# Performance work log

Hardware: AMD Instinct MI355X
Metric: run time of the kernel (lower is better)

## Reference

```python
import jax, jax.numpy as jnp
import numpy as np

N = 100000   # nodes
E = 1600000  # edges (avg degree 16)
D_IN = 128
H = 256
D_OUT = 128


def setup_inputs() -> dict:
    key = jax.random.key(0)
    ks = jax.random.split(key, 12)

    def lin_w(k, fan_in, fan_out):
        # torch nn.Linear-style uniform init
        bound = 1.0 / np.sqrt(fan_in)
        return jax.random.uniform(k, (fan_in, fan_out), jnp.float32, -bound, bound)

    return {
        "in_feat": jax.random.normal(ks[0], (N, D_IN), jnp.float32),
        "src": jax.random.randint(ks[1], (E,), 0, N, jnp.int32),
        "dst": jax.random.randint(ks[2], (E,), 0, N, jnp.int32),
        "Wc0": lin_w(ks[3], D_IN, H), "bc0": jnp.zeros((H,), jnp.float32),
        "Wc1": lin_w(ks[4], H, H),    "bc1": jnp.zeros((H,), jnp.float32),
        "Wc2": lin_w(ks[5], H, D_OUT),"bc2": jnp.zeros((D_OUT,), jnp.float32),
        "Wr0": lin_w(ks[6], D_OUT, H),"br0": jnp.zeros((H,), jnp.float32),
        "Wr1": lin_w(ks[7], H, H),    "br1": jnp.zeros((H,), jnp.float32),
        "Wr2": lin_w(ks[8], H, D_IN), "br2": jnp.zeros((D_IN,), jnp.float32),
    }


def _graph_conv(h, src, dst, W, b):
    """DGL GraphConv, norm='both': D_out^{-1/2} A D_in^{-1/2} h W + b."""
    ones = jnp.ones(src.shape[0], h.dtype)
    out_deg = jnp.clip(jax.ops.segment_sum(ones, src, num_segments=N), 1.0)
    in_deg = jnp.clip(jax.ops.segment_sum(ones, dst, num_segments=N), 1.0)
    h = h * (out_deg ** -0.5)[:, None]
    h = h @ W                                    # transform before aggregate
    h = jax.ops.segment_sum(h[src], dst, num_segments=N)  # SpMM aggregation
    return h * (in_deg ** -0.5)[:, None] + b


def reference(in_feat, src, dst, Wc0, bc0, Wc1, bc1, Wc2, bc2,
              Wr0, br0, Wr1, br1, Wr2, br2):
    h = jnp.tanh(_graph_conv(in_feat, src, dst, Wc0, bc0))
    h = jnp.tanh(_graph_conv(h, src, dst, Wc1, bc1))
    h = jax.nn.softmax(_graph_conv(h, src, dst, Wc2, bc2), axis=1)
    r = jnp.tanh(h @ Wr0 + br0)
    r = jnp.tanh(r @ Wr1 + br1)
    r = jax.nn.softmax(r @ Wr2 + br2, axis=1)
    return (h, r)
```

## Files before the change

kernel.cpp:

```cpp
#include <hip/hip_runtime.h>

typedef __attribute__((ext_vector_type(8))) short short8;
typedef __attribute__((ext_vector_type(4))) float f32x4;

__device__ __forceinline__ ushort f2bf(float v) {
    unsigned u = __builtin_bit_cast(unsigned, v);
    unsigned r = (u + 0x7FFFu + ((u >> 16) & 1u)) >> 16;
    return (ushort)r;
}
__device__ __forceinline__ float lo16(unsigned p) { return __builtin_bit_cast(float, p << 16); }
__device__ __forceinline__ float hi16(unsigned p) { return __builtin_bit_cast(float, p & 0xFFFF0000u); }

__device__ __forceinline__ float fast_tanh(float x) {
    float cx = fminf(fmaxf(x, -9.f), 9.f);
    float e = __expf(2.f * cx);
    return (e - 1.f) / (e + 1.f);
}

__device__ __forceinline__ void async16(const void* g, void* l) {
    __builtin_amdgcn_global_load_lds(
        (const __attribute__((address_space(1))) unsigned*)g,
        (__attribute__((address_space(3))) unsigned*)l, 16, 0, 0);
}

#define BSHIFT 9
#define CHUNK 4096

__global__ __launch_bounds__(256) void bucket_count(const int* __restrict__ src,
        const int* __restrict__ dst, int* __restrict__ gbc,
        int* __restrict__ outc, int E) {
    __shared__ int cnt[256];
    int t = threadIdx.x;
    cnt[t] = 0;
    __syncthreads();
    int start = blockIdx.x * CHUNK;
    int n = E - start; if (n > CHUNK) n = CHUNK;
#pragma unroll
    for (int k = 0; k < CHUNK / 256; ++k) {
        int i = t + k * 256;
        if (i < n) {
            atomicAdd(&cnt[dst[start + i] >> BSHIFT], 1);
            atomicAdd(&outc[src[start + i]], 1);
        }
    }
    __syncthreads();
    if (cnt[t]) atomicAdd(&gbc[t], cnt[t]);
}

__global__ void scan_buckets(const int* __restrict__ gbc, int* __restrict__ bucketBase,
                             int* __restrict__ pairCursor, int* __restrict__ roff,
                             int N, int E) {
    __shared__ int s[256];
    int t = threadIdx.x;
    int v = gbc[t];
    s[t] = v; __syncthreads();
    for (int o = 1; o < 256; o <<= 1) {
        int y = (t >= o) ? s[t - o] : 0;
        __syncthreads();
        s[t] += y;
        __syncthreads();
    }
    int excl = s[t] - v;
    bucketBase[t] = excl;
    pairCursor[t] = excl;
    if (t == 255) bucketBase[256] = s[255];
    if (t == 0) roff[N] = E;
}

__global__ __launch_bounds__(256) void part_scatter(const int* __restrict__ src,
        const int* __restrict__ dst, int* __restrict__ pairCursor,
        uint2* __restrict__ pairs, int E) {
    __shared__ int cnt[256];
    __shared__ int base[256];
    int t = threadIdx.x;
    cnt[t] = 0;
    __syncthreads();
    int start = blockIdx.x * CHUNK;
    int n = E - start; if (n > CHUNK) n = CHUNK;
    int sv[CHUNK / 256], dv[CHUNK / 256], rk[CHUNK / 256], bk[CHUNK / 256];
#pragma unroll
    for (int k = 0; k < CHUNK / 256; ++k) {
        int i = t + k * 256;
        if (i < n) {
            sv[k] = src[start + i];
            dv[k] = dst[start + i];
            bk[k] = dv[k] >> BSHIFT;
            rk[k] = atomicAdd(&cnt[bk[k]], 1);
        } else bk[k] = -1;
    }
    __syncthreads();
    base[t] = cnt[t] ? atomicAdd(&pairCursor[t], cnt[t]) : 0;
    __syncthreads();
#pragma unroll
    for (int k = 0; k < CHUNK / 256; ++k)
        if (bk[k] >= 0) pairs[base[bk[k]] + rk[k]] = make_uint2((unsigned)sv[k], (unsigned)dv[k]);
}

__global__ __launch_bounds__(256) void build_bucket(const uint2* __restrict__ pairs,
        const int* __restrict__ bucketBase, int* __restrict__ roff,
        float* __restrict__ sIn, int* __restrict__ csr, int N) {
    __shared__ int cnt[512];
    __shared__ int cur[512];
    __shared__ int ss[256];
    int b = blockIdx.x;
    int t = threadIdx.x;
    int lo = b << BSHIFT;
    int s0 = bucketBase[b], s1 = bucketBase[b + 1];
    cnt[t] = 0; cnt[t + 256] = 0;
    __syncthreads();
    for (int j = s0 + t; j < s1; j += 256)
        atomicAdd(&cnt[pairs[j].y - lo], 1);
    __syncthreads();
    int c0 = cnt[2 * t], c1 = cnt[2 * t + 1];
    ss[t] = c0 + c1; __syncthreads();
    for (int o = 1; o < 256; o <<= 1) {
        int y = (t >= o) ? ss[t - o] : 0;
        __syncthreads();
        ss[t] += y;
        __syncthreads();
    }
    int eb = ss[t] - (c0 + c1);
    int p0 = s0 + eb, p1 = s0 + eb + c0;
    cur[2 * t] = p0; cur[2 * t + 1] = p1;
    int n0 = lo + 2 * t, n1 = n0 + 1;
    if (n0 < N) { roff[n0] = p0; sIn[n0] = rsqrtf((float)(c0 > 0 ? c0 : 1)); }
    if (n1 < N) { roff[n1] = p1; sIn[n1] = rsqrtf((float)(c1 > 0 ? c1 : 1)); }
    __syncthreads();
    for (int j = s0 + t; j < s1; j += 256) {
        uint2 p = pairs[j];
        int pos = atomicAdd(&cur[p.y - lo], 1);
        csr[pos] = (int)p.x;
    }
}

__global__ void convw(const float* w0, const float* w1, const float* w2,
                      const float* w3, const float* w4, const float* w5,
                      ushort* __restrict__ Wt) {
    int i = blockIdx.x * 256 + threadIdx.x;
    int base, Km, Nm; const float* W;
    if      (i < 32768)  { base = 0;      Km = 128; Nm = 256; W = w0; }
    else if (i < 98304)  { base = 32768;  Km = 256; Nm = 256; W = w1; }
    else if (i < 131072) { base = 98304;  Km = 256; Nm = 128; W = w2; }
    else if (i < 163840) { base = 131072; Km = 128; Nm = 256; W = w3; }
    else if (i < 229376) { base = 163840; Km = 256; Nm = 256; W = w4; }
    else                 { base = 229376; Km = 256; Nm = 128; W = w5; }
    int l = i - base;
    int k = l / Nm, n = l % Nm;
    Wt[base + n * Km + k] = f2bf(W[l]);
}

__global__ void prescale(const float* __restrict__ x, const int* __restrict__ outc,
                         ushort* __restrict__ o, float* __restrict__ sOut,
                         int total ) {
    int i = blockIdx.x * 256 + threadIdx.x;
    if (i >= total) return;
    int row = i >> 5;
    int oc = outc[row]; if (oc < 1) oc = 1;
    float s = rsqrtf((float)oc);
    if ((i & 31) == 0) sOut[row] = s;
    float4 v = ((const float4*)x)[i];
    ushort4 r;
    r.x = f2bf(v.x * s); r.y = f2bf(v.y * s);
    r.z = f2bf(v.z * s); r.w = f2bf(v.w * s);
    ((ushort4*)o)[i] = r;
}

__global__ __launch_bounds__(256) void agg128(const ushort* __restrict__ F,
        const int* __restrict__ csr, const int* __restrict__ roff,
        const float* __restrict__ sIn, ushort* __restrict__ out, int N) {
    int w = blockIdx.x * 4 + (threadIdx.x >> 6);
    if (w >= N) return;
    int lane = threadIdx.x & 63;
    int b = roff[w], e = roff[w + 1];
    float a0 = 0.f, a1 = 0.f;
    const ushort* base = F + lane * 2;
    int i = b;
    for (; i + 4 <= e; i += 4) {
        int s0 = csr[i], s1 = csr[i + 1], s2 = csr[i + 2], s3 = csr[i + 3];
        unsigned p0 = *(const unsigned*)(base + (size_t)s0 * 128);
        unsigned p1 = *(const unsigned*)(base + (size_t)s1 * 128);
        unsigned p2 = *(const unsigned*)(base + (size_t)s2 * 128);
        unsigned p3 = *(const unsigned*)(base + (size_t)s3 * 128);
        a0 += lo16(p0) + lo16(p1) + lo16(p2) + lo16(p3);
        a1 += hi16(p0) + hi16(p1) + hi16(p2) + hi16(p3);
    }
    for (; i < e; ++i) {
        unsigned p = *(const unsigned*)(base + (size_t)csr[i] * 128);
        a0 += lo16(p); a1 += hi16(p);
    }
    float s = sIn[w];
    ushort2 o2; o2.x = f2bf(a0 * s); o2.y = f2bf(a1 * s);
    *(ushort2*)(out + (size_t)w * 128 + lane * 2) = o2;
}

__global__ __launch_bounds__(256) void agg256(const ushort* __restrict__ F,
        const int* __restrict__ csr, const int* __restrict__ roff,
        const float* __restrict__ sIn, ushort* __restrict__ out, int N) {
    int w = blockIdx.x * 4 + (threadIdx.x >> 6);
    if (w >= N) return;
    int lane = threadIdx.x & 63;
    int b = roff[w], e = roff[w + 1];
    float a0 = 0.f, a1 = 0.f, a2 = 0.f, a3 = 0.f;
    const ushort* base = F + lane * 4;
    int i = b;
    for (; i + 4 <= e; i += 4) {
        int s0 = csr[i], s1 = csr[i + 1], s2 = csr[i + 2], s3 = csr[i + 3];
        uint2 p0 = *(const uint2*)(base + (size_t)s0 * 256);
        uint2 p1 = *(const uint2*)(base + (size_t)s1 * 256);
        uint2 p2 = *(const uint2*)(base + (size_t)s2 * 256);
        uint2 p3 = *(const uint2*)(base + (size_t)s3 * 256);
        a0 += lo16(p0.x) + lo16(p1.x) + lo16(p2.x) + lo16(p3.x);
        a1 += hi16(p0.x) + hi16(p1.x) + hi16(p2.x) + hi16(p3.x);
        a2 += lo16(p0.y) + lo16(p1.y) + lo16(p2.y) + lo16(p3.y);
        a3 += hi16(p0.y) + hi16(p1.y) + hi16(p2.y) + hi16(p3.y);
    }
    for (; i < e; ++i) {
        uint2 p = *(const uint2*)(base + (size_t)csr[i] * 256);
        a0 += lo16(p.x); a1 += hi16(p.x); a2 += lo16(p.y); a3 += hi16(p.y);
    }
    float s = sIn[w];
    ushort4 o4;
    o4.x = f2bf(a0 * s); o4.y = f2bf(a1 * s);
    o4.z = f2bf(a2 * s); o4.w = f2bf(a3 * s);
    *(ushort4*)(out + (size_t)w * 256 + lane * 4) = o4;
}

__global__ __launch_bounds__(256) void agg_softmax(const ushort* __restrict__ F,
        const int* __restrict__ csr, const int* __restrict__ roff,
        const float* __restrict__ sIn, const float* __restrict__ bias,
        float* __restrict__ outh, ushort* __restrict__ outb, int N) {
    int w = blockIdx.x * 4 + (threadIdx.x >> 6);
    if (w >= N) return;
    int lane = threadIdx.x & 63;
    int b = roff[w], e = roff[w + 1];
    float a0 = 0.f, a1 = 0.f;
    const ushort* base = F + lane * 2;
    int i = b;
    for (; i + 4 <= e; i += 4) {
        int s0 = csr[i], s1 = csr[i + 1], s2 = csr[i + 2], s3 = csr[i + 3];
        unsigned p0 = *(const unsigned*)(base + (size_t)s0 * 128);
        unsigned p1 = *(const unsigned*)(base + (size_t)s1 * 128);
        unsigned p2 = *(const unsigned*)(base + (size_t)s2 * 128);
        unsigned p3 = *(const unsigned*)(base + (size_t)s3 * 128);
        a0 += lo16(p0) + lo16(p1) + lo16(p2) + lo16(p3);
        a1 += hi16(p0) + hi16(p1) + hi16(p2) + hi16(p3);
    }
    for (; i < e; ++i) {
        unsigned p = *(const unsigned*)(base + (size_t)csr[i] * 128);
        a0 += lo16(p); a1 += hi16(p);
    }
    float s = sIn[w];
    float2 bb = *(const float2*)(bias + lane * 2);
    float l0 = a0 * s + bb.x, l1 = a1 * s + bb.y;
    float m = fmaxf(l0, l1);
    for (int o = 32; o; o >>= 1) m = fmaxf(m, __shfl_xor(m, o, 64));
    float e0 = __expf(l0 - m), e1 = __expf(l1 - m);
    float sm = e0 + e1;
    for (int o = 32; o; o >>= 1) sm += __shfl_xor(sm, o, 64);
    float inv = 1.f / sm;
    float r0 = e0 * inv, r1 = e1 * inv;
    float2 fo; fo.x = r0; fo.y = r1;
    *(float2*)(outh + (size_t)w * 128 + lane * 2) = fo;
    ushort2 o2; o2.x = f2bf(r0); o2.y = f2bf(r1);
    *(ushort2*)(outb + (size_t)w * 128 + lane * 2) = o2;
}

__global__ __launch_bounds__(256) void softmax_r(const float* __restrict__ L,
                                                 float* __restrict__ out, int N) {
    int w = blockIdx.x * 4 + (threadIdx.x >> 6);
    if (w >= N) return;
    int lane = threadIdx.x & 63;
    const float* row = L + (size_t)w * 128;
    float l0 = row[lane], l1 = row[lane + 64];
    float m = fmaxf(l0, l1);
    for (int o = 32; o; o >>= 1) m = fmaxf(m, __shfl_xor(m, o, 64));
    float e0 = __expf(l0 - m), e1 = __expf(l1 - m);
    float sm = e0 + e1;
    for (int o = 32; o; o >>= 1) sm += __shfl_xor(sm, o, 64);
    float inv = 1.f / sm;
    out[(size_t)w * 128 + lane] = e0 * inv;
    out[(size_t)w * 128 + 64 + lane] = e1 * inv;
}

template <int MODE>
__global__ __launch_bounds__(256) void gemm_kernel(
        const ushort* __restrict__ A, const ushort* __restrict__ Wt,
        const float* __restrict__ bias, const float* __restrict__ rowscale,
        void* __restrict__ out, int M, int K, int Nn) {
    __shared__ ushort ldsA[128 * 64];
    __shared__ ushort ldsB[128 * 64];
    const int tid = threadIdx.x;
    const int lane = tid & 63;
    const int wid = tid >> 6;
    const int rowbase = blockIdx.x * 128;
    const int colbase = blockIdx.y * 128;
    const int wr = (wid >> 1) * 64;
    const int wc = (wid & 1) * 64;

    f32x4 acc[4][4];
#pragma unroll
    for (int i = 0; i < 4; ++i)
#pragma unroll
        for (int j = 0; j < 4; ++j) acc[i][j] = (f32x4){0.f, 0.f, 0.f, 0.f};

    const int sr = lane >> 3;
    const int sp = lane & 7;

    for (int kt = 0; kt < K; kt += 64) {
        __syncthreads();
#pragma unroll
        for (int it = 0; it < 4; ++it) {
            int rl = wid * 32 + it * 8 + sr;
            int grow = rowbase + rl; if (grow > M - 1) grow = M - 1;
            int gca = kt + ((sp ^ (rl & 7)) << 3);
            async16(A + (size_t)grow * K + gca, (char*)ldsA + (wid * 32 + it * 8) * 128);
            int gn = colbase + rl;
            int gcb = kt + ((sp ^ (rl & 7)) << 3);
            async16(Wt + (size_t)gn * K + gcb, (char*)ldsB + (wid * 32 + it * 8) * 128);
        }
        __syncthreads();
        const int l15 = lane & 15, l4 = lane >> 4;
#pragma unroll
        for (int ks = 0; ks < 2; ++ks) {
            short8 af[4], bfr[4];
#pragma unroll
            for (int rt = 0; rt < 4; ++rt) {
                int r = wr + rt * 16 + l15;
                int slot = (ks * 4 + l4) ^ (r & 7);
                af[rt] = *(const short8*)&ldsA[r * 64 + slot * 8];
            }
#pragma unroll
            for (int ct = 0; ct < 4; ++ct) {
                int n = wc + ct * 16 + l15;
                int slot = (ks * 4 + l4) ^ (n & 7);
                bfr[ct] = *(const short8*)&ldsB[n * 64 + slot * 8];
            }
#pragma unroll
            for (int rt = 0; rt < 4; ++rt)
#pragma unroll
                for (int ct = 0; ct < 4; ++ct)
                    acc[rt][ct] = __builtin_amdgcn_mfma_f32_16x16x32_bf16(
                        af[rt], bfr[ct], acc[rt][ct], 0, 0, 0);
        }
    }

    const int l15 = lane & 15, l4 = lane >> 4;
    float bv[4];
#pragma unroll
    for (int ct = 0; ct < 4; ++ct)
        bv[ct] = (MODE != 1 && bias) ? bias[colbase + wc + ct * 16 + l15] : 0.f;
#pragma unroll
    for (int rt = 0; rt < 4; ++rt) {
#pragma unroll
        for (int rg = 0; rg < 4; ++rg) {
            int row = rowbase + wr + rt * 16 + l4 * 4 + rg;
            if (row >= M) continue;
            float sc = 1.f;
            if (MODE == 0 && rowscale) sc = rowscale[row];
#pragma unroll
            for (int ct = 0; ct < 4; ++ct) {
                int col = colbase + wc + ct * 16 + l15;
                float v = acc[rt][ct][rg] + bv[ct];
                if (MODE == 0) v = fast_tanh(v) * sc;
                if (MODE <= 1)
                    ((ushort*)out)[(size_t)row * Nn + col] = f2bf(v);
                else
                    ((float*)out)[(size_t)row * Nn + col] = v;
            }
        }
    }
}

extern "C" void kernel_launch(void* const* d_in, const int* in_sizes, int n_in,
                              void* d_out, int out_size, void* d_ws, size_t ws_size,
                              hipStream_t stream) {
    (void)n_in; (void)out_size; (void)ws_size;
    const float* in_feat = (const float*)d_in[0];
    const int*   src     = (const int*)d_in[1];
    const int*   dstp    = (const int*)d_in[2];
    const float* Wc0 = (const float*)d_in[3];  const float* bc0 = (const float*)d_in[4];
    const float* Wc1 = (const float*)d_in[5];  const float* bc1 = (const float*)d_in[6];
    const float* Wc2 = (const float*)d_in[7];  const float* bc2 = (const float*)d_in[8];
    const float* Wr0 = (const float*)d_in[9];  const float* br0 = (const float*)d_in[10];
    const float* Wr1 = (const float*)d_in[11]; const float* br1 = (const float*)d_in[12];
    const float* Wr2 = (const float*)d_in[13]; const float* br2 = (const float*)d_in[14];

    const int N = in_sizes[0] / 128;
    const int E = in_sizes[1];
    const int numBuckets = (N + ((1 << BSHIFT) - 1)) >> BSHIFT;

    char* ws = (char*)d_ws;
    size_t off = 0;
    auto alloc = [&](size_t bytes) -> char* {
        char* p = ws + off;
        off += (bytes + 255) & ~(size_t)255;
        return p;
    };
    char* S1 = alloc((size_t)N * 256 * 2);
    char* S2 = alloc((size_t)N * 256 * 2);
    int* csr    = (int*)alloc((size_t)E * 4);
    int* roff   = (int*)alloc((size_t)(N + 1) * 4);
    int* outc   = (int*)alloc((size_t)N * 4);
    float* sOut = (float*)alloc((size_t)N * 4);
    float* sIn  = (float*)alloc((size_t)N * 4);
    ushort* Wt  = (ushort*)alloc(262144 * 2);
    int* gbc        = (int*)alloc(256 * 4);
    int* bucketBase = (int*)alloc(257 * 4);
    int* pairCursor = (int*)alloc(256 * 4);
    uint2* pairs = (uint2*)S2;

    hipMemsetAsync(outc, 0, (size_t)N * 4, stream);
    hipMemsetAsync(gbc, 0, 256 * 4, stream);

    int nblk = (E + CHUNK - 1) / CHUNK;
    bucket_count<<<nblk, 256, 0, stream>>>(src, dstp, gbc, outc, E);
    scan_buckets<<<1, 256, 0, stream>>>(gbc, bucketBase, pairCursor, roff, N, E);
    part_scatter<<<nblk, 256, 0, stream>>>(src, dstp, pairCursor, pairs, E);
    build_bucket<<<numBuckets, 256, 0, stream>>>(pairs, bucketBase, roff, sIn, csr, N);

    convw<<<262144 / 256, 256, 0, stream>>>(Wc0, Wc1, Wc2, Wr0, Wr1, Wr2, Wt);

    ushort* Xs = (ushort*)S1;
    prescale<<<(N * 32 + 255) / 256, 256, 0, stream>>>(in_feat, outc, Xs, sOut, N * 32);

    int aggGrid = (N + 3) / 4;
    dim3 g2((N + 127) / 128, 2), g1((N + 127) / 128, 1);

    ushort* A0 = (ushort*)S2;
    agg128<<<aggGrid, 256, 0, stream>>>(Xs, csr, roff, sIn, A0, N);
    ushort* B1 = (ushort*)S1;
    gemm_kernel<0><<<g2, 256, 0, stream>>>(A0, Wt, bc0, sOut, B1, N, 128, 256);
    ushort* A1 = (ushort*)S2;
    agg256<<<aggGrid, 256, 0, stream>>>(B1, csr, roff, sIn, A1, N);
    ushort* B2 = (ushort*)S1;
    gemm_kernel<0><<<g2, 256, 0, stream>>>(A1, Wt + 32768, bc1, sOut, B2, N, 256, 256);
    ushort* T3 = (ushort*)S2;
    gemm_kernel<1><<<g1, 256, 0, stream>>>(B2, Wt + 98304, nullptr, nullptr, T3, N, 256, 128);
    float* outh = (float*)d_out;
    ushort* Hbf = (ushort*)S1;
    agg_softmax<<<aggGrid, 256, 0, stream>>>(T3, csr, roff, sIn, bc2, outh, Hbf, N);
    ushort* R1 = (ushort*)S2;
    gemm_kernel<0><<<g2, 256, 0, stream>>>(Hbf, Wt + 131072, br0, nullptr, R1, N, 128, 256);
    ushort* R2 = (ushort*)S1;
    gemm_kernel<0><<<g2, 256, 0, stream>>>(R1, Wt + 163840, br1, nullptr, R2, N, 256, 256);
    float* logits = (float*)S2;
    gemm_kernel<2><<<g1, 256, 0, stream>>>(R2, Wt + 229376, br2, nullptr, logits, N, 256, 128);
    softmax_r<<<aggGrid, 256, 0, stream>>>(logits, outh + (size_t)N * 128, N);
}
```

Measured before the change: 766.9 us.

## Store features in column-sliced layout so SpMM gathers fit per-slice in cache

Prescale and the first two GEMM epilogues now write bf16 features in a sliced layout of 16-column slabs, each holding all N rows. The new agg_sliced kernel processes one slice at a time, with 16 lanes splitting each row's edges and a shuffle reduction at the end. Each slab is about 3.2 MB, so a slice's random gathers should stay resident in L2/MALL instead of thrashing across the full feature matrix. The trade-off is 32-byte gathers, more blocks, and a cross-lane reduction per row, and the GEMM A loads and epilogue stores must handle the strided sliced addressing.

```diff
diff --git a/kernel.cpp b/kernel.cpp
--- a/kernel.cpp
+++ b/kernel.cpp
@@ -151,78 +151,70 @@
 
 __global__ void prescale(const float* __restrict__ x, const int* __restrict__ outc,
                          ushort* __restrict__ o, float* __restrict__ sOut,
-                         int total ) {
+                         int N, int total ) {
     int i = blockIdx.x * 256 + threadIdx.x;
     if (i >= total) return;
     int row = i >> 5;
+    int g = i & 31;
     int oc = outc[row]; if (oc < 1) oc = 1;
     float s = rsqrtf((float)oc);
-    if ((i & 31) == 0) sOut[row] = s;
+    if (g == 0) sOut[row] = s;
     float4 v = ((const float4*)x)[i];
     ushort4 r;
     r.x = f2bf(v.x * s); r.y = f2bf(v.y * s);
     r.z = f2bf(v.z * s); r.w = f2bf(v.w * s);
-    ((ushort4*)o)[i] = r;
-}
-
-__global__ __launch_bounds__(256) void agg128(const ushort* __restrict__ F,
+    *(ushort4*)(o + ((size_t)(g >> 2) * N + row) * 16 + (g & 3) * 4) = r;
+}
+
+template <int NS>
+__global__ __launch_bounds__(256) void agg_sliced(const ushort* __restrict__ F,
         const int* __restrict__ csr, const int* __restrict__ roff,
-        const float* __restrict__ sIn, ushort* __restrict__ out, int N) {
-    int w = blockIdx.x * 4 + (threadIdx.x >> 6);
-    if (w >= N) return;
+        const float* __restrict__ sIn, ushort* __restrict__ out,
+        int N, int nch, int rpc) {
+    int bid = blockIdx.x;
+    int slice, chunk;
+    if (NS == 16) {
+        int half = 8 * nch;
+        int phase = (bid >= half) ? 1 : 0;
+        int r = bid - phase * half;
+        slice = (r & 7) + 8 * phase;
+        chunk = r >> 3;
+    } else {
+        slice = bid & 7;
+        chunk = bid >> 3;
+    }
+    const ushort* Fs = F + (size_t)slice * N * 16;
+    ushort* Os = out + (size_t)slice * N * 16;
     int lane = threadIdx.x & 63;
-    int b = roff[w], e = roff[w + 1];
-    float a0 = 0.f, a1 = 0.f;
-    const ushort* base = F + lane * 2;
-    int i = b;
-    for (; i + 4 <= e; i += 4) {
-        int s0 = csr[i], s1 = csr[i + 1], s2 = csr[i + 2], s3 = csr[i + 3];
-        unsigned p0 = *(const unsigned*)(base + (size_t)s0 * 128);
-        unsigned p1 = *(const unsigned*)(base + (size_t)s1 * 128);
-        unsigned p2 = *(const unsigned*)(base + (size_t)s2 * 128);
-        unsigned p3 = *(const unsigned*)(base + (size_t)s3 * 128);
-        a0 += lo16(p0) + lo16(p1) + lo16(p2) + lo16(p3);
-        a1 += hi16(p0) + hi16(p1) + hi16(p2) + hi16(p3);
-    }
-    for (; i < e; ++i) {
-        unsigned p = *(const unsigned*)(base + (size_t)csr[i] * 128);
-        a0 += lo16(p); a1 += hi16(p);
-    }
-    float s = sIn[w];
-    ushort2 o2; o2.x = f2bf(a0 * s); o2.y = f2bf(a1 * s);
-    *(ushort2*)(out + (size_t)w * 128 + lane * 2) = o2;
-}
-
-__global__ __launch_bounds__(256) void agg256(const ushort* __restrict__ F,
-        const int* __restrict__ csr, const int* __restrict__ roff,
-        const float* __restrict__ sIn, ushort* __restrict__ out, int N) {
-    int w = blockIdx.x * 4 + (threadIdx.x >> 6);
-    if (w >= N) return;
-    int lane = threadIdx.x & 63;
-    int b = roff[w], e = roff[w + 1];
-    float a0 = 0.f, a1 = 0.f, a2 = 0.f, a3 = 0.f;
-    const ushort* base = F + lane * 4;
-    int i = b;
-    for (; i + 4 <= e; i += 4) {
-        int s0 = csr[i], s1 = csr[i + 1], s2 = csr[i + 2], s3 = csr[i + 3];
-        uint2 p0 = *(const uint2*)(base + (size_t)s0 * 256);
-        uint2 p1 = *(const uint2*)(base + (size_t)s1 * 256);
-        uint2 p2 = *(const uint2*)(base + (size_t)s2 * 256);
-        uint2 p3 = *(const uint2*)(base + (size_t)s3 * 256);
-        a0 += lo16(p0.x) + lo16(p1.x) + lo16(p2.x) + lo16(p3.x);
-        a1 += hi16(p0.x) + hi16(p1.x) + hi16(p2.x) + hi16(p3.x);
-        a2 += lo16(p0.y) + lo16(p1.y) + lo16(p2.y) + lo16(p3.y);
-        a3 += hi16(p0.y) + hi16(p1.y) + hi16(p2.y) + hi16(p3.y);
-    }
-    for (; i < e; ++i) {
-        uint2 p = *(const uint2*)(base + (size_t)csr[i] * 256);
-        a0 += lo16(p.x); a1 += hi16(p.x); a2 += lo16(p.y); a3 += hi16(p.y);
-    }
-    float s = sIn[w];
-    ushort4 o4;
-    o4.x = f2bf(a0 * s); o4.y = f2bf(a1 * s);
-    o4.z = f2bf(a2 * s); o4.w = f2bf(a3 * s);
-    *(ushort4*)(out + (size_t)w * 256 + lane * 4) = o4;
+    int wv = threadIdx.x >> 6;
+    int eg = lane >> 2;
+    int part = lane & 3;
+    int r0 = chunk * rpc;
+    int r1 = r0 + rpc; if (r1 > N) r1 = N;
+    for (int w = r0 + wv; w < r1; w += 4) {
+        int b = roff[w], e = roff[w + 1];
+        float a0 = 0.f, a1 = 0.f, a2 = 0.f, a3 = 0.f;
+        for (int i = b + eg; i < e; i += 16) {
+            int s = csr[i];
+            uint2 p = *(const uint2*)(Fs + (size_t)s * 16 + part * 4);
+            a0 += lo16(p.x); a1 += hi16(p.x);
+            a2 += lo16(p.y); a3 += hi16(p.y);
+        }
+#pragma unroll
+        for (int o = 4; o <= 32; o <<= 1) {
+            a0 += __shfl_xor(a0, o, 64);
+            a1 += __shfl_xor(a1, o, 64);
+            a2 += __shfl_xor(a2, o, 64);
+            a3 += __shfl_xor(a3, o, 64);
+        }
+        if (lane < 4) {
+            float s = sIn[w];
+            ushort4 o4;
+            o4.x = f2bf(a0 * s); o4.y = f2bf(a1 * s);
+            o4.z = f2bf(a2 * s); o4.w = f2bf(a3 * s);
+            *(ushort4*)(Os + (size_t)w * 16 + part * 4) = o4;
+        }
+    }
 }
 
 __global__ __launch_bounds__(256) void agg_softmax(const ushort* __restrict__ F,
@@ -282,7 +274,7 @@
     out[(size_t)w * 128 + 64 + lane] = e1 * inv;
 }
 
-template <int MODE>
+template <int MODE, int ASL, int OSL>
 __global__ __launch_bounds__(256) void gemm_kernel(
         const ushort* __restrict__ A, const ushort* __restrict__ Wt,
         const float* __restrict__ bias, const float* __restrict__ rowscale,
@@ -313,7 +305,10 @@
             int rl = wid * 32 + it * 8 + sr;
             int grow = rowbase + rl; if (grow > M - 1) grow = M - 1;
             int gca = kt + ((sp ^ (rl & 7)) << 3);
-            async16(A + (size_t)grow * K + gca, (char*)ldsA + (wid * 32 + it * 8) * 128);
+            const ushort* ga = ASL
+                ? A + ((size_t)(gca >> 4) * M + grow) * 16 + (gca & 15)
+                : A + (size_t)grow * K + gca;
+            async16(ga, (char*)ldsA + (wid * 32 + it * 8) * 128);
             int gn = colbase + rl;
             int gcb = kt + ((sp ^ (rl & 7)) << 3);
             async16(Wt + (size_t)gn * K + gcb, (char*)ldsB + (wid * 32 + it * 8) * 128);
@@ -362,10 +357,14 @@
                 int col = colbase + wc + ct * 16 + l15;
                 float v = acc[rt][ct][rg] + bv[ct];
                 if (MODE == 0) v = fast_tanh(v) * sc;
-                if (MODE <= 1)
-                    ((ushort*)out)[(size_t)row * Nn + col] = f2bf(v);
-                else
+                if (MODE <= 1) {
+                    size_t idx = OSL
+                        ? ((size_t)(col >> 4) * M + row) * 16 + (col & 15)
+                        : (size_t)row * Nn + col;
+                    ((ushort*)out)[idx] = f2bf(v);
+                } else {
                     ((float*)out)[(size_t)row * Nn + col] = v;
+                }
             }
         }
     }
@@ -421,29 +420,31 @@
     convw<<<262144 / 256, 256, 0, stream>>>(Wc0, Wc1, Wc2, Wr0, Wr1, Wr2, Wt);
 
     ushort* Xs = (ushort*)S1;
-    prescale<<<(N * 32 + 255) / 256, 256, 0, stream>>>(in_feat, outc, Xs, sOut, N * 32);
-
+    prescale<<<(N * 32 + 255) / 256, 256, 0, stream>>>(in_feat, outc, Xs, sOut, N, N * 32);
+
+    const int nch = 2048;
+    const int rpc = (N + nch - 1) / nch;
     int aggGrid = (N + 3) / 4;
     dim3 g2((N + 127) / 128, 2), g1((N + 127) / 128, 1);
 
     ushort* A0 = (ushort*)S2;
-    agg128<<<aggGrid, 256, 0, stream>>>(Xs, csr, roff, sIn, A0, N);
+    agg_sliced<8><<<8 * nch, 256, 0, stream>>>(Xs, csr, roff, sIn, A0, N, nch, rpc);
     ushort* B1 = (ushort*)S1;
-    gemm_kernel<0><<<g2, 256, 0, stream>>>(A0, Wt, bc0, sOut, B1, N, 128, 256);
+    gemm_kernel<0, 1, 1><<<g2, 256, 0, stream>>>(A0, Wt, bc0, sOut, B1, N, 128, 256);
     ushort* A1 = (ushort*)S2;
-    agg256<<<aggGrid, 256, 0, stream>>>(B1, csr, roff, sIn, A1, N);
+    agg_sliced<16><<<16 * nch, 256, 0, stream>>>(B1, csr, roff, sIn, A1, N, nch, rpc);
     ushort* B2 = (ushort*)S1;
-    gemm_kernel<0><<<g2, 256, 0, stream>>>(A1, Wt + 32768, bc1, sOut, B2, N, 256, 256);
+    gemm_kernel<0, 1, 0><<<g2, 256, 0, stream>>>(A1, Wt + 32768, bc1, sOut, B2, N, 256, 256);
     ushort* T3 = (ushort*)S2;
-    gemm_kernel<1><<<g1, 256, 0, stream>>>(B2, Wt + 98304, nullptr, nullptr, T3, N, 256, 128);
+    gemm_kernel<1, 0, 0><<<g1, 256, 0, stream>>>(B2, Wt + 98304, nullptr, nullptr, T3, N, 256, 128);
     float* outh = (float*)d_out;
     ushort* Hbf = (ushort*)S1;
     agg_softmax<<<aggGrid, 256, 0, stream>>>(T3, csr, roff, sIn, bc2, outh, Hbf, N);
     ushort* R1 = (ushort*)S2;
-    gemm_kernel<0><<<g2, 256, 0, stream>>>(Hbf, Wt + 131072, br0, nullptr, R1, N, 128, 256);
+    gemm_kernel<0, 0, 0><<<g2, 256, 0, stream>>>(Hbf, Wt + 131072, br0, nullptr, R1, N, 128, 256);
     ushort* R2 = (ushort*)S1;
-    gemm_kernel<0><<<g2, 256, 0, stream>>>(R1, Wt + 163840, br1, nullptr, R2, N, 256, 256);
+    gemm_kernel<0, 0, 0><<<g2, 256, 0, stream>>>(R1, Wt + 163840, br1, nullptr, R2, N, 256, 256);
     float* logits = (float*)S2;
-    gemm_kernel<2><<<g1, 256, 0, stream>>>(R2, Wt + 229376, br2, nullptr, logits, N, 256, 128);
+    gemm_kernel<2, 0, 0><<<g1, 256, 0, stream>>>(R2, Wt + 229376, br2, nullptr, logits, N, 256, 128);
     softmax_r<<<aggGrid, 256, 0, stream>>>(logits, outh + (size_t)N * 128, N);
 }
```

After: 1.102 ms. 43.7% more time.

## Replace LDS-staged GEMM with register-direct MFMA GEMM and compile-time K

Applied to the files above, without the earlier changes.

The shared-memory tiled GEMM, which used async global-to-LDS loads and two barriers per K step, is replaced by a kernel in which each wavefront loads its A and B fragments straight from global memory into registers. Each wave computes a 32x128 output tile. K becomes a template parameter so the loop can be unrolled, and the grid is reordered so column blocks vary fastest, letting neighbouring blocks share A rows in cache. This removes LDS traffic and synchronisation but drops data reuse across waves, so each wave rereads the weight tile from global memory or L2.

```diff
diff --git a/kernel.cpp b/kernel.cpp
--- a/kernel.cpp
+++ b/kernel.cpp
@@ -15,12 +15,6 @@
     float cx = fminf(fmaxf(x, -9.f), 9.f);
     float e = __expf(2.f * cx);
     return (e - 1.f) / (e + 1.f);
-}
-
-__device__ __forceinline__ void async16(const void* g, void* l) {
-    __builtin_amdgcn_global_load_lds(
-        (const __attribute__((address_space(1))) unsigned*)g,
-        (__attribute__((address_space(3))) unsigned*)l, 16, 0, 0);
 }
 
 #define BSHIFT 9
@@ -282,84 +276,57 @@
     out[(size_t)w * 128 + 64 + lane] = e1 * inv;
 }
 
-template <int MODE>
-__global__ __launch_bounds__(256) void gemm_kernel(
+template <int MODE, int K>
+__global__ __launch_bounds__(256) void gemm_reg(
         const ushort* __restrict__ A, const ushort* __restrict__ Wt,
         const float* __restrict__ bias, const float* __restrict__ rowscale,
-        void* __restrict__ out, int M, int K, int Nn) {
-    __shared__ ushort ldsA[128 * 64];
-    __shared__ ushort ldsB[128 * 64];
+        void* __restrict__ out, int M, int Nn) {
     const int tid = threadIdx.x;
     const int lane = tid & 63;
     const int wid = tid >> 6;
-    const int rowbase = blockIdx.x * 128;
-    const int colbase = blockIdx.y * 128;
-    const int wr = (wid >> 1) * 64;
-    const int wc = (wid & 1) * 64;
-
-    f32x4 acc[4][4];
-#pragma unroll
-    for (int i = 0; i < 4; ++i)
-#pragma unroll
-        for (int j = 0; j < 4; ++j) acc[i][j] = (f32x4){0.f, 0.f, 0.f, 0.f};
-
-    const int sr = lane >> 3;
-    const int sp = lane & 7;
-
-    for (int kt = 0; kt < K; kt += 64) {
-        __syncthreads();
-#pragma unroll
-        for (int it = 0; it < 4; ++it) {
-            int rl = wid * 32 + it * 8 + sr;
-            int grow = rowbase + rl; if (grow > M - 1) grow = M - 1;
-            int gca = kt + ((sp ^ (rl & 7)) << 3);
-            async16(A + (size_t)grow * K + gca, (char*)ldsA + (wid * 32 + it * 8) * 128);
-            int gn = colbase + rl;
-            int gcb = kt + ((sp ^ (rl & 7)) << 3);
-            async16(Wt + (size_t)gn * K + gcb, (char*)ldsB + (wid * 32 + it * 8) * 128);
+    const int l15 = lane & 15, l4 = lane >> 4;
+    const int rowbase = blockIdx.y * 128 + wid * 32;
+    const int colbase = blockIdx.x * 128;
+
+    f32x4 acc[2][8];
+#pragma unroll
+    for (int i = 0; i < 2; ++i)
+#pragma unroll
+        for (int j = 0; j < 8; ++j) acc[i][j] = (f32x4){0.f, 0.f, 0.f, 0.f};
+
+    int r0 = rowbase + l15;      if (r0 > M - 1) r0 = M - 1;
+    int r1 = rowbase + 16 + l15; if (r1 > M - 1) r1 = M - 1;
+    const ushort* a0 = A + (size_t)r0 * K + l4 * 8;
+    const ushort* a1 = A + (size_t)r1 * K + l4 * 8;
+    const ushort* b0 = Wt + (size_t)(colbase + l15) * K + l4 * 8;
+
+#pragma unroll 4
+    for (int kt = 0; kt < K; kt += 32) {
+        short8 af0 = *(const short8*)(a0 + kt);
+        short8 af1 = *(const short8*)(a1 + kt);
+#pragma unroll
+        for (int ct = 0; ct < 8; ++ct) {
+            short8 bf = *(const short8*)(b0 + (size_t)ct * 16 * K + kt);
+            acc[0][ct] = __builtin_amdgcn_mfma_f32_16x16x32_bf16(af0, bf, acc[0][ct], 0, 0, 0);
+            acc[1][ct] = __builtin_amdgcn_mfma_f32_16x16x32_bf16(af1, bf, acc[1][ct], 0, 0, 0);
         }
-        __syncthreads();
-        const int l15 = lane & 15, l4 = lane >> 4;
-#pragma unroll
-        for (int ks = 0; ks < 2; ++ks) {
-            short8 af[4], bfr[4];
-#pragma unroll
-            for (int rt = 0; rt < 4; ++rt) {
-                int r = wr + rt * 16 + l15;
-                int slot = (ks * 4 + l4) ^ (r & 7);
-                af[rt] = *(const short8*)&ldsA[r * 64 + slot * 8];
-            }
-#pragma unroll
-            for (int ct = 0; ct < 4; ++ct) {
-                int n = wc + ct * 16 + l15;
-                int slot = (ks * 4 + l4) ^ (n & 7);
-                bfr[ct] = *(const short8*)&ldsB[n * 64 + slot * 8];
-            }
-#pragma unroll
-            for (int rt = 0; rt < 4; ++rt)
-#pragma unroll
-                for (int ct = 0; ct < 4; ++ct)
-                    acc[rt][ct] = __builtin_amdgcn_mfma_f32_16x16x32_bf16(
-                        af[rt], bfr[ct], acc[rt][ct], 0, 0, 0);
-        }
-    }
-
-    const int l15 = lane & 15, l4 = lane >> 4;
-    float bv[4];
-#pragma unroll
-    for (int ct = 0; ct < 4; ++ct)
-        bv[ct] = (MODE != 1 && bias) ? bias[colbase + wc + ct * 16 + l15] : 0.f;
-#pragma unroll
-    for (int rt = 0; rt < 4; ++rt) {
+    }
+
+    float bv[8];
+#pragma unroll
+    for (int ct = 0; ct < 8; ++ct)
+        bv[ct] = (MODE != 1 && bias) ? bias[colbase + ct * 16 + l15] : 0.f;
+#pragma unroll
+    for (int rt = 0; rt < 2; ++rt) {
 #pragma unroll
         for (int rg = 0; rg < 4; ++rg) {
-            int row = rowbase + wr + rt * 16 + l4 * 4 + rg;
+            int row = rowbase + rt * 16 + l4 * 4 + rg;
             if (row >= M) continue;
             float sc = 1.f;
             if (MODE == 0 && rowscale) sc = rowscale[row];
 #pragma unroll
-            for (int ct = 0; ct < 4; ++ct) {
-                int col = colbase + wc + ct * 16 + l15;
+            for (int ct = 0; ct < 8; ++ct) {
+                int col = colbase + ct * 16 + l15;
                 float v = acc[rt][ct][rg] + bv[ct];
                 if (MODE == 0) v = fast_tanh(v) * sc;
                 if (MODE <= 1)
@@ -424,26 +391,27 @@
     prescale<<<(N * 32 + 255) / 256, 256, 0, stream>>>(in_feat, outc, Xs, sOut, N * 32);
 
     int aggGrid = (N + 3) / 4;
-    dim3 g2((N + 127) / 128, 2), g1((N + 127) / 128, 1);
+    int rowblk = (N + 127) / 128;
+    dim3 g2(2, rowblk), g1(1, rowblk);
 
     ushort* A0 = (ushort*)S2;
     agg128<<<aggGrid, 256, 0, stream>>>(Xs, csr, roff, sIn, A0, N);
     ushort* B1 = (ushort*)S1;
-    gemm_kernel<0><<<g2, 256, 0, stream>>>(A0, Wt, bc0, sOut, B1, N, 128, 256);
+    gemm_reg<0, 128><<<g2, 256, 0, stream>>>(A0, Wt, bc0, sOut, B1, N, 256);
     ushort* A1 = (ushort*)S2;
     agg256<<<aggGrid, 256, 0, stream>>>(B1, csr, roff, sIn, A1, N);
     ushort* B2 = (ushort*)S1;
-    gemm_kernel<0><<<g2, 256, 0, stream>>>(A1, Wt + 32768, bc1, sOut, B2, N, 256, 256);
+    gemm_reg<0, 256><<<g2, 256, 0, stream>>>(A1, Wt + 32768, bc1, sOut, B2, N, 256);
     ushort* T3 = (ushort*)S2;
-    gemm_kernel<1><<<g1, 256, 0, stream>>>(B2, Wt + 98304, nullptr, nullptr, T3, N, 256, 128);
+    gemm_reg<1, 256><<<g1, 256, 0, stream>>>(B2, Wt + 98304, nullptr, nullptr, T3, N, 128);
     float* outh = (float*)d_out;
     ushort* Hbf = (ushort*)S1;
     agg_softmax<<<aggGrid, 256, 0, stream>>>(T3, csr, roff, sIn, bc2, outh, Hbf, N);
     ushort* R1 = (ushort*)S2;
-    gemm_kernel<0><<<g2, 256, 0, stream>>>(Hbf, Wt + 131072, br0, nullptr, R1, N, 128, 256);
+    gemm_reg<0, 128><<<g2, 256, 0, stream>>>(Hbf, Wt + 131072, br0, nullptr, R1, N, 256);
     ushort* R2 = (ushort*)S1;
-    gemm_kernel<0><<<g2, 256, 0, stream>>>(R1, Wt + 163840, br1, nullptr, R2, N, 256, 256);
+    gemm_reg<0, 256><<<g2, 256, 0, stream>>>(R1, Wt + 163840, br1, nullptr, R2, N, 256);
     float* logits = (float*)S2;
-    gemm_kernel<2><<<g1, 256, 0, stream>>>(R2, Wt + 229376, br2, nullptr, logits, N, 256, 128);
+    gemm_reg<2, 256><<<g1, 256, 0, stream>>>(R2, Wt + 229376, br2, nullptr, logits, N, 128);
     softmax_r<<<aggGrid, 256, 0, stream>>>(logits, outh + (size_t)N * 128, N);
 }
```

Measured after the change: 925.6 us. 1.21x slower.
